# Kernel tuning notes

Measured on AMD Instinct MI355X. Metric: run time of the kernel, lower is better.

The kernel has to match this reference:

```python
import math
import jax, jax.numpy as jnp
import numpy as np

FS = 16000          # sample rate implied by undefined global `fs` in source
NFFT = 320          # win_len == frame_len
HOP = 160           # inc
C_SOUND = 340.0
ARRAY_DIS = 0.027


def _steering(F, n_ch, angle_deg):
    # h = conj(exp(-1j*2*pi*f_k * sensor * d * sin(theta)/c)) -> exp(+1j*...)
    f_k = np.arange(F) * (FS // NFFT)                      # integer bins * 50 Hz
    delay = np.arange(n_ch) * ARRAY_DIS * np.sin(angle_deg * np.pi / 180.0) / C_SOUND
    h = np.exp(1j * 2.0 * np.pi * f_k[:, None] * delay[None, :]).astype(np.complex64)
    return jnp.asarray(h)[..., None]                       # [F, C, 1]


def _stft(x, window):
    # x: [B, C, L] float32; torch.stft defaults: center=True, reflect pad
    pad = NFFT // 2
    xp = jnp.pad(x, ((0, 0), (0, 0), (pad, pad)), mode='reflect')
    T = 1 + (xp.shape[-1] - NFFT) // HOP
    idx = jnp.arange(T)[:, None] * HOP + jnp.arange(NFFT)[None, :]
    frames = xp[:, :, idx] * window                        # [B, C, T, NFFT]
    return jnp.fft.rfft(frames, axis=-1)                   # [B, C, T, F] complex64


def _istft(S):
    # S: [B, F, T] complex; torch.istft with default (rectangular) window
    frames = jnp.fft.irfft(jnp.moveaxis(S, 1, 2), n=NFFT, axis=-1)  # [B, T, NFFT]
    B, T, _ = frames.shape
    out_len = NFFT + HOP * (T - 1)
    idx = jnp.arange(T)[:, None] * HOP + jnp.arange(NFFT)[None, :]
    out = jnp.zeros((B, out_len), frames.dtype).at[:, idx].add(frames)
    wsum = jnp.zeros((out_len,), frames.dtype).at[idx.reshape(-1)].add(1.0)
    pad = NFFT // 2
    return (out / wsum)[:, pad:-pad]


def setup_inputs() -> dict:
    key = jax.random.key(0)
    B, L, C = 8, 160000, 4
    mc_wav = jax.random.normal(key, (B, L, C), dtype=jnp.float32)
    # torch.kaiser_window(320, periodic=True, beta=6)
    window = jnp.asarray(np.kaiser(NFFT + 1, 6.0)[:NFFT].astype(np.float32))
    return {"mc_wav": mc_wav, "window": window}


def reference(mc_wav, window):
    B, L, C = mc_wav.shape
    # pre-normalize: remove DC per channel, scale by per-batch global max-abs
    x = mc_wav - jnp.mean(mc_wav, axis=1, keepdims=True)
    x = x / jnp.max(jnp.abs(x), axis=(1, 2), keepdims=True)
    x = jnp.transpose(x, (0, 2, 1))                        # [B, C, L]

    S = _stft(x, window)                                   # [B, C, T, F]
    F = S.shape[-1]
    Xs = jnp.transpose(S, (2, 0, 3, 1))                    # [T, B, F, C] frames-first
    T = Xs.shape[0]

    h1 = _steering(F, C, -40.0)                            # [F, C, 1]
    h2 = _steering(F, C, 40.0)
    eye = jnp.eye(C, dtype=S.dtype)

    def beam(invR, h, X):
        num = jnp.einsum('bfcd,fdo->bfco', invR, h)        # invR @ h  [B,F,C,1]
        den = jnp.einsum('fco,bfco->bf', h.conj(), num)    # h^H invR h
        w = num[..., 0] / den[..., None]                   # [B, F, C]
        return jnp.einsum('bfc,bfc->bf', w.conj(), X)      # w^H X

    def step(RXX, inp):
        X, first = inp                                     # X: [B, F, C]
        outer = jnp.einsum('bfc,bfd->bfcd', X, X.conj())
        RXX = jnp.where(first, outer, 0.05 * RXX + 0.95 * outer)
        tr = jnp.trace(RXX, axis1=-2, axis2=-1)[..., None, None]
        invR = jnp.linalg.inv(RXX + (tr / C) * eye)        # diag-loaded inverse
        return RXX, (beam(invR, h1, X), beam(invR, h2, X))

    RXX0 = jnp.zeros((B, F, C, C), dtype=S.dtype)
    firsts = jnp.arange(T) == 0
    _, (s1, s2) = jax.lax.scan(step, RXX0, (Xs, firsts))

    S1 = jnp.transpose(s1, (1, 2, 0))                      # [B, F, T]
    S2 = jnp.transpose(s2, (1, 2, 0))
    return _istft(S1), _istft(S2)
```

## Files before the change

kernel.cpp:

```cpp
#include <hip/hip_runtime.h>
#include <hip/hip_bf16.h>
#include <math.h>

#define BB 8
#define LL 160000
#define CC 4
#define NFFT 320
#define HOP 160
#define FB 161
#define TT 1001
#define TP 1024
#define RBLK 128
#define PI_D 3.14159265358979323846
#define NPAD 160320

#define KWARM 4

#define GM 16016
#define KSEC 352
#define LDK 704
#define KT 11
#define NGEN (2*FB*CC + 384*640 + NFFT*LDK)

typedef __attribute__((ext_vector_type(8))) short bf16x8;
typedef __attribute__((ext_vector_type(4))) float f32x4;

__device__ __forceinline__ void ldsdma16(const short* g, short* l){
    __builtin_amdgcn_global_load_lds((const __attribute__((address_space(1))) void*)g,
                                     (__attribute__((address_space(3))) void*)l, 16, 0, 0);
}

__device__ __forceinline__ float2 cmulf(float2 a, float2 b){
    return make_float2(a.x*b.x - a.y*b.y, a.x*b.y + a.y*b.x);
}
__device__ __forceinline__ float2 cmulcj(float2 a, float2 b){
    return make_float2(a.x*b.x + a.y*b.y, a.y*b.x - a.x*b.y);
}
__device__ __forceinline__ float2 cjmul(float2 a, float2 b){
    return make_float2(a.x*b.x + a.y*b.y, a.x*b.y - a.y*b.x);
}
__device__ __forceinline__ float2 csub(float2 a, float2 b){ return make_float2(a.x-b.x, a.y-b.y); }
__device__ __forceinline__ float2 cscale(float2 a, float s){ return make_float2(a.x*s, a.y*s); }
__device__ __forceinline__ float2 cdivf(float2 a, float2 b){
    float inv = 1.0f/(b.x*b.x + b.y*b.y);
    return make_float2((a.x*b.x + a.y*b.y)*inv, (a.y*b.x - a.x*b.y)*inv);
}
__device__ __forceinline__ short bf_hi(float v){
    __hip_bfloat16 h = __float2bfloat16(v);
    short s; __builtin_memcpy(&s, &h, 2); return s;
}
__device__ __forceinline__ short bf_lo(float v){
    __hip_bfloat16 h = __float2bfloat16(v);
    float r = v - __bfloat162float(h);
    __hip_bfloat16 l = __float2bfloat16(r);
    short s; __builtin_memcpy(&s, &l, 2); return s;
}

__global__ __launch_bounds__(256) void k_genstats(const float* __restrict__ in, float* __restrict__ part,
        const float* __restrict__ win, float* __restrict__ htab,
        short* __restrict__ Bts, short* __restrict__ Bt){
    __shared__ float4 s4[256];
    __shared__ float4 mn4[256];
    __shared__ float4 mx4[256];
    int tid = threadIdx.x;
    if (blockIdx.x < BB*RBLK){
        int b = blockIdx.x / RBLK, chunk = blockIdx.x % RBLK;
        const float4* p = (const float4*)(in + (size_t)b*LL*CC);
        const int per = LL / RBLK;
        int start = chunk*per;
        float4 s  = make_float4(0.f,0.f,0.f,0.f);
        float4 mn = make_float4( 3.4e38f, 3.4e38f, 3.4e38f, 3.4e38f);
        float4 mx = make_float4(-3.4e38f,-3.4e38f,-3.4e38f,-3.4e38f);
        for (int i = start + tid; i < start + per; i += 256){
            float4 v = p[i];
            s.x += v.x; s.y += v.y; s.z += v.z; s.w += v.w;
            mn.x = fminf(mn.x, v.x); mn.y = fminf(mn.y, v.y); mn.z = fminf(mn.z, v.z); mn.w = fminf(mn.w, v.w);
            mx.x = fmaxf(mx.x, v.x); mx.y = fmaxf(mx.y, v.y); mx.z = fmaxf(mx.z, v.z); mx.w = fmaxf(mx.w, v.w);
        }
        s4[tid] = s; mn4[tid] = mn; mx4[tid] = mx;
        __syncthreads();
        for (int st = 128; st >= 1; st >>= 1){
            if (tid < st){
                float4 a = s4[tid], c = s4[tid+st];
                s4[tid] = make_float4(a.x+c.x, a.y+c.y, a.z+c.z, a.w+c.w);
                float4 d = mn4[tid], e = mn4[tid+st];
                mn4[tid] = make_float4(fminf(d.x,e.x), fminf(d.y,e.y), fminf(d.z,e.z), fminf(d.w,e.w));
                float4 f = mx4[tid], g = mx4[tid+st];
                mx4[tid] = make_float4(fmaxf(f.x,g.x), fmaxf(f.y,g.y), fmaxf(f.z,g.z), fmaxf(f.w,g.w));
            }
            __syncthreads();
        }
        if (tid == 0){
            float* dst = part + (size_t)(b*RBLK + chunk)*12;
            float4 a = s4[0], d = mn4[0], f = mx4[0];
            dst[0]=a.x; dst[1]=a.y; dst[2]=a.z; dst[3]=a.w;
            dst[4]=d.x; dst[5]=d.y; dst[6]=d.z; dst[7]=d.w;
            dst[8]=f.x; dst[9]=f.y; dst[10]=f.z; dst[11]=f.w;
        }
        return;
    }
    int gid = (blockIdx.x - BB*RBLK)*256 + tid;
    const float W0 = (float)(2.0*PI_D/320.0);
    if (gid < 2*FB*CC){
        int i = gid;
        int c = i & 3;
        int k = (i >> 2) % FB;
        int m = i / (FB*CC);
        double coef = 2.0*PI_D*50.0*0.027*sin(40.0*PI_D/180.0)/340.0;
        double sgn = (m == 0) ? -1.0 : 1.0;
        double ph = sgn*coef*(double)k*(double)c;
        double s, c2;
        sincos(ph, &s, &c2);
        ((float2*)htab)[i] = make_float2((float)c2, (float)s);
        return;
    }
    gid -= 2*FB*CC;
    if (gid < 384*640){
        int col = gid / 640, kk = gid % 640;
        int n = (kk >= 320) ? kk - 320 : kk;
        int sec = (kk >= 320) ? 1 : 0;
        float v = 0.f;
        if (col < 2*FB){
            int k = col >> 1;
            int mr = (k*n) % 320;
            float s, co; sincosf(W0*(float)mr, &s, &co);
            v = win[n] * ((col & 1) ? -s : co);
        }
        Bts[gid] = sec ? bf_lo(v) : bf_hi(v);
        return;
    }
    gid -= 384*640;
    if (gid < NFFT*LDK){
        int n = gid / LDK, kk = gid % LDK;
        int sec = (kk >= KSEC) ? 1 : 0;
        int kk2 = kk - (sec ? KSEC : 0);
        float v = 0.f;
        if (kk2 < 2*FB){
            int bin = kk2 >> 1;
            float c = ((bin == 0 || bin == 160) ? 1.0f : 2.0f) * (1.0f/320.0f);
            int mr = (bin*n) % 320;
            float s, co; sincosf(W0*(float)mr, &s, &co);
            v = (kk2 & 1) ? -c*s : c*co;
        }
        Bt[(size_t)n*LDK + kk] = sec ? bf_lo(v) : bf_hi(v);
    }
}

__global__ __launch_bounds__(128) void k_stats2(const float* __restrict__ part,
                                                float* __restrict__ mean, float* __restrict__ invmax){
    __shared__ float4 s4[128];
    __shared__ float4 mn4[128];
    __shared__ float4 mx4[128];
    int b = blockIdx.x, tid = threadIdx.x;
    const float* src = part + (size_t)(b*RBLK + tid)*12;
    s4[tid]  = make_float4(src[0], src[1], src[2], src[3]);
    mn4[tid] = make_float4(src[4], src[5], src[6], src[7]);
    mx4[tid] = make_float4(src[8], src[9], src[10], src[11]);
    __syncthreads();
    for (int st = 64; st >= 1; st >>= 1){
        if (tid < st){
            float4 a = s4[tid], c = s4[tid+st];
            s4[tid] = make_float4(a.x+c.x, a.y+c.y, a.z+c.z, a.w+c.w);
            float4 d = mn4[tid], e = mn4[tid+st];
            mn4[tid] = make_float4(fminf(d.x,e.x), fminf(d.y,e.y), fminf(d.z,e.z), fminf(d.w,e.w));
            float4 f = mx4[tid], g = mx4[tid+st];
            mx4[tid] = make_float4(fmaxf(f.x,g.x), fmaxf(f.y,g.y), fmaxf(f.z,g.z), fmaxf(f.w,g.w));
        }
        __syncthreads();
    }
    if (tid == 0){
        float4 sum = s4[0], mn = mn4[0], mx = mx4[0];
        float m0 = sum.x*(1.0f/LL), m1 = sum.y*(1.0f/LL), m2 = sum.z*(1.0f/LL), m3 = sum.w*(1.0f/LL);
        mean[b*4+0]=m0; mean[b*4+1]=m1; mean[b*4+2]=m2; mean[b*4+3]=m3;
        float a0 = fmaxf(mx.x - m0, m0 - mn.x);
        float a1 = fmaxf(mx.y - m1, m1 - mn.y);
        float a2 = fmaxf(mx.z - m2, m2 - mn.z);
        float a3 = fmaxf(mx.w - m3, m3 - mn.w);
        invmax[b] = 1.0f / fmaxf(fmaxf(a0, a1), fmaxf(a2, a3));
    }
}

__global__ __launch_bounds__(256) void k_anorm(const float* __restrict__ in,
        const float* __restrict__ mean, const float* __restrict__ invmax,
        short* __restrict__ Ahi, short* __restrict__ Alo){
    int gid = blockIdx.x*256 + threadIdx.x;
    if (gid >= BB*(NPAD/8)) return;
    int p8 = gid % (NPAD/8);
    int b  = gid / (NPAD/8);
    float4 mc = *(const float4*)&mean[b*4];
    float iv = invmax[b];
    const float4* px = (const float4*)(in + (size_t)b*LL*CC);
    bf16x8 h0{}, h1{}, h2{}, h3{}, l0{}, l1{}, l2{}, l3{};
    #pragma unroll
    for (int j = 0; j < 8; ++j){
        int p = p8*8 + j - 160;
        int m2 = p < 0 ? -p : (p >= LL ? 2*LL - 2 - p : p);
        float4 v = px[m2];
        float v0 = (v.x - mc.x)*iv, v1 = (v.y - mc.y)*iv;
        float v2 = (v.z - mc.z)*iv, v3 = (v.w - mc.w)*iv;
        h0[j] = bf_hi(v0); l0[j] = bf_lo(v0);
        h1[j] = bf_hi(v1); l1[j] = bf_lo(v1);
        h2[j] = bf_hi(v2); l2[j] = bf_lo(v2);
        h3[j] = bf_hi(v3); l3[j] = bf_lo(v3);
    }
    size_t o = (size_t)(b*4)*NPAD + (size_t)p8*8;
    *(bf16x8*)&Ahi[o]          = h0;  *(bf16x8*)&Alo[o]          = l0;
    *(bf16x8*)&Ahi[o +   NPAD] = h1;  *(bf16x8*)&Alo[o +   NPAD] = l1;
    *(bf16x8*)&Ahi[o + 2*NPAD] = h2;  *(bf16x8*)&Alo[o + 2*NPAD] = l2;
    *(bf16x8*)&Ahi[o + 3*NPAD] = h3;  *(bf16x8*)&Alo[o + 3*NPAD] = l3;
}

__global__ __launch_bounds__(512, 4) void k_gstft(const short* __restrict__ Ahi, const short* __restrict__ Alo,
        const short* __restrict__ Bts, float* __restrict__ S){
    __shared__ short stage[40960];
    int tid = threadIdx.x;
    int row0 = blockIdx.x*128;
    int col0 = blockIdx.y*192;
    int b  = row0 >> 12;
    int t0 = (row0 & 4095) >> 2;
    int wave = tid >> 6, lane = tid & 63;
    int wm = wave >> 1, wn = wave & 1;
    int l15 = lane & 15, quad = lane >> 4;
    int chunk = (tid & 3) ^ ((tid >> 3) & 3);
    int tq4 = tid >> 2;
    int rowA = tq4;
    int tls = t0 + (rowA >> 2); if (tls >= TT) tls = TT - 1;
    size_t gao = (size_t)(b*4 + (rowA & 3))*NPAD + (size_t)tls*160 + chunk*8;
    const short* src0 = Ahi + gao;
    const short* src1 = Alo + gao;
    const short* src2 = Bts + (size_t)(col0 + tq4)*640 + chunk*8;
    const short* src3 = (tid < 256)
        ? Bts + (size_t)(col0 + 128 + tq4)*640 + chunk*8
        : Bts + (size_t)(col0 + ((tid - 256) >> 2))*640 + 320 + chunk*8;
    const short* src4 = Bts + (size_t)(col0 + 64 + tq4)*640 + 320 + chunk*8;
    short* lw = stage + wave*512;
    int sw  = (l15 >> 1) & 3;
    int c0r = (quad ^ sw) * 8;
    int ra0 = (wm*32 + l15)*32 + c0r;
    int rbB = (wn*96 + l15)*32 + c0r;
    f32x4 c00 = {0.f,0.f,0.f,0.f}, c01 = c00, c02 = c00, c03 = c00, c04 = c00, c05 = c00;
    f32x4 c10 = c00, c11 = c00, c12 = c00, c13 = c00, c14 = c00, c15 = c00;

    #define STG(kt_, off_) do{ int ko_ = (kt_)*32; \
        ldsdma16(src0 + ko_, lw + (off_));          \
        ldsdma16(src1 + ko_, lw + (off_) + 4096);   \
        ldsdma16(src2 + ko_, lw + (off_) + 8192);   \
        ldsdma16(src3 + ko_, lw + (off_) + 12288);  \
        ldsdma16(src4 + ko_, lw + (off_) + 16384);  \
    }while(0)

    STG(0, 0);
    STG(1, 20480);
    #pragma unroll
    for (int kt = 0; kt < 10; ++kt){
        int offc = (kt & 1) ? 20480 : 0;
        if (kt < 9) asm volatile("s_waitcnt vmcnt(5)" ::: "memory");
        else        asm volatile("s_waitcnt vmcnt(0)" ::: "memory");
        __builtin_amdgcn_s_barrier();
        bf16x8 a0h = *(bf16x8*)&stage[offc + ra0];
        bf16x8 a1h = *(bf16x8*)&stage[offc + ra0 + 512];
        bf16x8 a0l = *(bf16x8*)&stage[offc + 4096 + ra0];
        bf16x8 a1l = *(bf16x8*)&stage[offc + 4096 + ra0 + 512];
        bf16x8 b0h = *(bf16x8*)&stage[offc + 8192 + rbB];
        bf16x8 b1h = *(bf16x8*)&stage[offc + 8192 + rbB + 512];
        bf16x8 b2h = *(bf16x8*)&stage[offc + 8192 + rbB + 1024];
        bf16x8 b3h = *(bf16x8*)&stage[offc + 8192 + rbB + 1536];
        bf16x8 b4h = *(bf16x8*)&stage[offc + 8192 + rbB + 2048];
        bf16x8 b5h = *(bf16x8*)&stage[offc + 8192 + rbB + 2560];
        c00 = __builtin_amdgcn_mfma_f32_16x16x32_bf16(a0h, b0h, c00, 0, 0, 0);
        c01 = __builtin_amdgcn_mfma_f32_16x16x32_bf16(a0h, b1h, c01, 0, 0, 0);
        c02 = __builtin_amdgcn_mfma_f32_16x16x32_bf16(a0h, b2h, c02, 0, 0, 0);
        c03 = __builtin_amdgcn_mfma_f32_16x16x32_bf16(a0h, b3h, c03, 0, 0, 0);
        c04 = __builtin_amdgcn_mfma_f32_16x16x32_bf16(a0h, b4h, c04, 0, 0, 0);
        c05 = __builtin_amdgcn_mfma_f32_16x16x32_bf16(a0h, b5h, c05, 0, 0, 0);
        c10 = __builtin_amdgcn_mfma_f32_16x16x32_bf16(a1h, b0h, c10, 0, 0, 0);
        c11 = __builtin_amdgcn_mfma_f32_16x16x32_bf16(a1h, b1h, c11, 0, 0, 0);
        c12 = __builtin_amdgcn_mfma_f32_16x16x32_bf16(a1h, b2h, c12, 0, 0, 0);
        c13 = __builtin_amdgcn_mfma_f32_16x16x32_bf16(a1h, b3h, c13, 0, 0, 0);
        c14 = __builtin_amdgcn_mfma_f32_16x16x32_bf16(a1h, b4h, c14, 0, 0, 0);
        c15 = __builtin_amdgcn_mfma_f32_16x16x32_bf16(a1h, b5h, c15, 0, 0, 0);
        c00 = __builtin_amdgcn_mfma_f32_16x16x32_bf16(a0l, b0h, c00, 0, 0, 0);
        c01 = __builtin_amdgcn_mfma_f32_16x16x32_bf16(a0l, b1h, c01, 0, 0, 0);
        c02 = __builtin_amdgcn_mfma_f32_16x16x32_bf16(a0l, b2h, c02, 0, 0, 0);
        c03 = __builtin_amdgcn_mfma_f32_16x16x32_bf16(a0l, b3h, c03, 0, 0, 0);
        c04 = __builtin_amdgcn_mfma_f32_16x16x32_bf16(a0l, b4h, c04, 0, 0, 0);
        c05 = __builtin_amdgcn_mfma_f32_16x16x32_bf16(a0l, b5h, c05, 0, 0, 0);
        c10 = __builtin_amdgcn_mfma_f32_16x16x32_bf16(a1l, b0h, c10, 0, 0, 0);
        c11 = __builtin_amdgcn_mfma_f32_16x16x32_bf16(a1l, b1h, c11, 0, 0, 0);
        c12 = __builtin_amdgcn_mfma_f32_16x16x32_bf16(a1l, b2h, c12, 0, 0, 0);
        c13 = __builtin_amdgcn_mfma_f32_16x16x32_bf16(a1l, b3h, c13, 0, 0, 0);
        c14 = __builtin_amdgcn_mfma_f32_16x16x32_bf16(a1l, b4h, c14, 0, 0, 0);
        c15 = __builtin_amdgcn_mfma_f32_16x16x32_bf16(a1l, b5h, c15, 0, 0, 0);
        bf16x8 b0l = *(bf16x8*)&stage[offc + 14336 + rbB];
        bf16x8 b1l = *(bf16x8*)&stage[offc + 14336 + rbB + 512];
        bf16x8 b2l = *(bf16x8*)&stage[offc + 14336 + rbB + 1024];
        bf16x8 b3l = *(bf16x8*)&stage[offc + 14336 + rbB + 1536];
        bf16x8 b4l = *(bf16x8*)&stage[offc + 14336 + rbB + 2048];
        bf16x8 b5l = *(bf16x8*)&stage[offc + 14336 + rbB + 2560];
        asm volatile("s_waitcnt lgkmcnt(0)" ::: "memory");
        __builtin_amdgcn_sched_barrier(0);
        __builtin_amdgcn_s_barrier();
        if (kt < 8) STG(kt+2, offc);
        c00 = __builtin_amdgcn_mfma_f32_16x16x32_bf16(a0h, b0l, c00, 0, 0, 0);
        c01 = __builtin_amdgcn_mfma_f32_16x16x32_bf16(a0h, b1l, c01, 0, 0, 0);
        c02 = __builtin_amdgcn_mfma_f32_16x16x32_bf16(a0h, b2l, c02, 0, 0, 0);
        c03 = __builtin_amdgcn_mfma_f32_16x16x32_bf16(a0h, b3l, c03, 0, 0, 0);
        c04 = __builtin_amdgcn_mfma_f32_16x16x32_bf16(a0h, b4l, c04, 0, 0, 0);
        c05 = __builtin_amdgcn_mfma_f32_16x16x32_bf16(a0h, b5l, c05, 0, 0, 0);
        c10 = __builtin_amdgcn_mfma_f32_16x16x32_bf16(a1h, b0l, c10, 0, 0, 0);
        c11 = __builtin_amdgcn_mfma_f32_16x16x32_bf16(a1h, b1l, c11, 0, 0, 0);
        c12 = __builtin_amdgcn_mfma_f32_16x16x32_bf16(a1h, b2l, c12, 0, 0, 0);
        c13 = __builtin_amdgcn_mfma_f32_16x16x32_bf16(a1h, b3l, c13, 0, 0, 0);
        c14 = __builtin_amdgcn_mfma_f32_16x16x32_bf16(a1h, b4l, c14, 0, 0, 0);
        c15 = __builtin_amdgcn_mfma_f32_16x16x32_bf16(a1h, b5l, c15, 0, 0, 0);
    }
    #undef STG
    int tq  = t0 + wm*8 + quad;
    int kgb = (col0 >> 1) + wn*48 + (l15 >> 1);
    int h   = l15 & 1;
    float4* S4 = (float4*)S;
    #define EPI(cf, i_, j_) do{ \
        int t = tq + 4*(i_); \
        int kg = kgb + 8*(j_); \
        if (t < TT && kg < FB){ \
            float p0 = __shfl_xor(cf[0], 1); \
            float p1 = __shfl_xor(cf[1], 1); \
            float p2 = __shfl_xor(cf[2], 1); \
            float p3 = __shfl_xor(cf[3], 1); \
            float4 v = h ? make_float4(p2, cf[2], p3, cf[3]) \
                         : make_float4(cf[0], p0, cf[1], p1); \
            S4[((size_t)((b*FB + kg)*2 + h))*TT + t] = v; \
        } \
    }while(0)
    EPI(c00, 0, 0); EPI(c01, 0, 1); EPI(c02, 0, 2); EPI(c03, 0, 3); EPI(c04, 0, 4); EPI(c05, 0, 5);
    EPI(c10, 1, 0); EPI(c11, 1, 1); EPI(c12, 1, 2); EPI(c13, 1, 3); EPI(c14, 1, 4); EPI(c15, 1, 5);
    #undef EPI
}

#define UPD(first) do{ \
    float aa = (first) ? 0.f : 0.05f; float wg = (first) ? 1.f : 0.95f; \
    float y0x=wg*x0.x, y0y=wg*x0.y, y1x=wg*x1.x, y1y=wg*x1.y; \
    float y2x=wg*x2.x, y2y=wg*x2.y, y3x=wg*x3.x, y3y=wg*x3.y; \
    d0 = aa*d0 + y0x*x0.x + y0y*x0.y; \
    d1 = aa*d1 + y1x*x1.x + y1y*x1.y; \
    d2 = aa*d2 + y2x*x2.x + y2y*x2.y; \
    d3 = aa*d3 + y3x*x3.x + y3y*x3.y; \
    r10.x = aa*r10.x + y1x*x0.x + y1y*x0.y;  r10.y = aa*r10.y + y1y*x0.x - y1x*x0.y; \
    r20.x = aa*r20.x + y2x*x0.x + y2y*x0.y;  r20.y = aa*r20.y + y2y*x0.x - y2x*x0.y; \
    r30.x = aa*r30.x + y3x*x0.x + y3y*x0.y;  r30.y = aa*r30.y + y3y*x0.x - y3x*x0.y; \
    r21.x = aa*r21.x + y2x*x1.x + y2y*x1.y;  r21.y = aa*r21.y + y2y*x1.x - y2x*x1.y; \
    r31.x = aa*r31.x + y3x*x1.x + y3y*x1.y;  r31.y = aa*r31.y + y3y*x1.x - y3x*x1.y; \
    r32.x = aa*r32.x + y3x*x2.x + y3y*x2.y;  r32.y = aa*r32.y + y3y*x2.x - y3x*x2.y; \
}while(0)

#define UPDQ do{ \
    d0 = 0.05f*d0 + x0.x*x0.x + x0.y*x0.y; \
    d1 = 0.05f*d1 + x1.x*x1.x + x1.y*x1.y; \
    d2 = 0.05f*d2 + x2.x*x2.x + x2.y*x2.y; \
    d3 = 0.05f*d3 + x3.x*x3.x + x3.y*x3.y; \
    r10.x = 0.05f*r10.x + x1.x*x0.x + x1.y*x0.y;  r10.y = 0.05f*r10.y + x1.y*x0.x - x1.x*x0.y; \
    r20.x = 0.05f*r20.x + x2.x*x0.x + x2.y*x0.y;  r20.y = 0.05f*r20.y + x2.y*x0.x - x2.x*x0.y; \
    r30.x = 0.05f*r30.x + x3.x*x0.x + x3.y*x0.y;  r30.y = 0.05f*r30.y + x3.y*x0.x - x3.x*x0.y; \
    r21.x = 0.05f*r21.x + x2.x*x1.x + x2.y*x1.y;  r21.y = 0.05f*r21.y + x2.y*x1.x - x2.x*x1.y; \
    r31.x = 0.05f*r31.x + x3.x*x1.x + x3.y*x1.y;  r31.y = 0.05f*r31.y + x3.y*x1.x - x3.x*x1.y; \
    r32.x = 0.05f*r32.x + x3.x*x2.x + x3.y*x2.y;  r32.y = 0.05f*r32.y + x3.y*x2.x - x3.x*x2.y; \
}while(0)

__global__ __launch_bounds__(512) void k_scan(const float* __restrict__ S, const float* __restrict__ htab,
                      short* __restrict__ S1, short* __restrict__ S2){
    __shared__ float4 tile[2016];
    int bf = blockIdx.x;
    int f  = bf % FB;
    int tid = threadIdx.x;
    const float4* P0 = (const float4*)S + (size_t)(bf*2)*TT;
    const float4* P1 = P0 + TT;
    for (int i = tid; i < 2*TT; i += 512){
        int tt = i >> 1;
        tile[i ^ ((i>>4)&7)] = (i & 1) ? P1[tt] : P0[tt];
    }
    __syncthreads();
    int t0 = tid*2;
    if (t0 < TT){
        const float2* hp = (const float2*)htab;
        float2 ha0 = hp[f*4+0], ha1 = hp[f*4+1], ha2 = hp[f*4+2], ha3 = hp[f*4+3];
        float2 hb0 = hp[(FB+f)*4+0], hb1 = hp[(FB+f)*4+1], hb2 = hp[(FB+f)*4+2], hb3 = hp[(FB+f)*4+3];
        float d0=0,d1=0,d2=0,d3=0;
        float2 r10={0,0}, r20={0,0}, r30={0,0}, r21={0,0}, r31={0,0}, r32={0,0};
        float2 x0, x1, x2, x3;
        #define LOADX(tau_) do{ int i0_ = 2*(tau_); \
            float4 v0_ = tile[i0_ ^ ((i0_>>4)&7)]; \
            float4 v1_ = tile[(i0_+1) ^ (((i0_+1)>>4)&7)]; \
            x0 = make_float2(v0_.x, v0_.y); x1 = make_float2(v0_.z, v0_.w); \
            x2 = make_float2(v1_.x, v1_.y); x3 = make_float2(v1_.z, v1_.w); \
        }while(0)
        bool qform = (t0 >= KWARM + 1);
        int ts = t0 - KWARM; if (ts < 0) ts = 0;
        if (qform){
            #pragma unroll
            for (int u = 0; u < KWARM; ++u){ LOADX(ts + u); UPDQ; }
        } else {
            for (int tau = 0; tau < t0; ++tau){ LOADX(tau); UPD(tau == 0); }
        }
        short4* S1g = (short4*)S1 + (size_t)bf*TT;
        short4* S2g = (short4*)S2 + (size_t)bf*TT;
        #pragma unroll
        for (int j = 0; j < 2; ++j){
            int t = t0 + j;
            if (t >= TT) break;
            LOADX(t);
            if (qform) UPDQ; else UPD(t == 0);
            float trc = d0 + d1 + d2 + d3;
            float lam = trc * 0.25f;
            float e0 = d0 + lam, e1 = d1 + lam, e2 = d2 + lam, e3 = d3 + lam;
            float detP = e0*e1 - (r10.x*r10.x + r10.y*r10.y);
            float2 w00 = csub(cscale(r20, e1), cmulf(r10, r21));
            float2 w01 = csub(cscale(r30, e1), cmulf(r10, r31));
            float2 w10 = csub(cscale(r21, e0), cjmul(r10, r20));
            float2 w11 = csub(cscale(r31, e0), cjmul(r10, r30));
            float2 va = cjmul(r30, w00), vb = cjmul(r31, w10);
            float2 V10 = make_float2(va.x + vb.x, -(va.y + vb.y));
            float reV00 = r20.x*w00.x + r20.y*w00.y + r21.x*w10.x + r21.y*w10.y;
            float reV11 = r30.x*w01.x + r30.y*w01.y + r31.x*w11.x + r31.y*w11.y;
            float t00 = detP*e2 - reV00;
            float t11 = detP*e3 - reV11;
            float2 t10 = csub(cscale(r32, detP), V10);
            float detT = t00*t11 - (t10.x*t10.x + t10.y*t10.y);
            #pragma unroll
            for (int m = 0; m < 2; ++m){
                float2 h0 = m ? hb0 : ha0;
                float2 h1 = m ? hb1 : ha1;
                float2 h2 = m ? hb2 : ha2;
                float2 h3 = m ? hb3 : ha3;
                float2 g0 = csub(cscale(h0, e1), cjmul(r10, h1));
                float2 g1 = csub(cscale(h1, e0), cmulf(r10, h0));
                float2 ta = cmulf(r20, g0), tb = cmulf(r21, g1);
                float2 hh0 = make_float2(detP*h2.x - ta.x - tb.x, detP*h2.y - ta.y - tb.y);
                ta = cmulf(r30, g0); tb = cmulf(r31, g1);
                float2 hh1 = make_float2(detP*h3.x - ta.x - tb.x, detP*h3.y - ta.y - tb.y);
                float2 y20 = csub(cscale(hh0, t11), cjmul(t10, hh1));
                float2 y21 = csub(cscale(hh1, t00), cmulf(t10, hh0));
                float2 u20 = cscale(y20, detP), u21 = cscale(y21, detP);
                ta = cmulcj(y20, r20); tb = cmulcj(y21, r30);
                float2 q0 = make_float2(detT*h0.x - ta.x - tb.x, detT*h0.y - ta.y - tb.y);
                ta = cmulcj(y20, r21); tb = cmulcj(y21, r31);
                float2 q1 = make_float2(detT*h1.x - ta.x - tb.x, detT*h1.y - ta.y - tb.y);
                float2 u10 = csub(cscale(q0, e1), cjmul(r10, q1));
                float2 u11 = csub(cscale(q1, e0), cmulf(r10, q0));
                float2 den = cjmul(h0, u10), tmp;
                tmp = cjmul(h1, u11); den.x += tmp.x; den.y += tmp.y;
                tmp = cjmul(h2, u20); den.x += tmp.x; den.y += tmp.y;
                tmp = cjmul(h3, u21); den.x += tmp.x; den.y += tmp.y;
                float2 num = cjmul(u10, x0);
                tmp = cjmul(u11, x1); num.x += tmp.x; num.y += tmp.y;
                tmp = cjmul(u20, x2); num.x += tmp.x; num.y += tmp.y;
                tmp = cjmul(u21, x3); num.x += tmp.x; num.y += tmp.y;
                float2 s = cdivf(num, make_float2(den.x, -den.y));
                short4 pk;
                pk.x = bf_hi(s.x); pk.y = bf_hi(s.y);
                pk.z = bf_lo(s.x); pk.w = bf_lo(s.y);
                if (m) S2g[t] = pk; else S1g[t] = pk;
            }
        }
        #undef LOADX
    }
}

__global__ __launch_bounds__(256) void k_pack(const short* __restrict__ S1, const short* __restrict__ S2,
                                              short* __restrict__ A){
    __shared__ short tile[32*708];
    int bid = blockIdx.x;
    int tb = bid & 31, rb = bid >> 5;
    int t0 = tb*32;
    int beam = rb >> 3, b = rb & 7;
    const short4* Sp = (const short4*)(beam ? S2 : S1) + (size_t)b*FB*TT;
    int tid = threadIdx.x;
    for (int idx = tid; idx < 32*176; idx += 256){
        int bin = idx >> 5, tq = idx & 31;
        int t = t0 + tq;
        short4 s = make_short4(0, 0, 0, 0);
        if (bin < FB && t < TT) s = Sp[(size_t)bin*TT + t];
        int c0 = 2*bin;
        tile[tq*708 + c0]            = s.x;
        tile[tq*708 + c0 + 1]        = s.y;
        tile[tq*708 + KSEC + c0]     = s.z;
        tile[tq*708 + KSEC + c0 + 1] = s.w;
    }
    __syncthreads();
    for (int idx = tid; idx < 32*176; idx += 256){
        int tq = idx / 176, k4 = idx % 176;
        int t = t0 + tq;
        if (t < TT)
            *(short4*)&A[(size_t)(rb*TT + t)*LDK + k4*4] = *(short4*)&tile[tq*708 + k4*4];
    }
}

__global__ __launch_bounds__(512, 4) void k_gemm(const short* __restrict__ A, const short* __restrict__ Bt,
                                                 float* __restrict__ C){
    __shared__ short sb2[24576];
    int tid = threadIdx.x;
    int row0 = blockIdx.y * 128;
    int col0 = blockIdx.x * 128;
    int wave = tid >> 6, lane = tid & 63;
    int wm = wave >> 1, wn = wave & 1;
    int l15 = lane & 15, quad = lane >> 4;
    bool wlive = (col0 + wn*64) < NFFT;
    int rowS  = wave*16 + (lane >> 2);
    int chunk = (lane & 3) ^ ((lane >> 3) & 3);
    int grS = row0 + rowS; if (grS >= GM) grS = GM - 1;
    int grB = col0 + rowS; if (grB >= NFFT) grB = NFFT - 1;
    const short* gA = A  + (size_t)grS*LDK + chunk*8;
    const short* gB = Bt + (size_t)grB*LDK + chunk*8;
    short* lA = sb2 + wave*512;
    int sw  = (l15 >> 1) & 3;
    int c0r = (quad ^ sw) * 8;
    int ra0 = (wm*32 + l15)*32 + c0r;
    int rb0 = (wn*64 + l15)*32 + c0r;
    f32x4 c00 = {0.f,0.f,0.f,0.f}, c01 = c00, c02 = c00, c03 = c00;
    f32x4 c10 = c00, c11 = c00, c12 = c00, c13 = c00;

    #define KOF(s_, ka_, kb_) { int sg_ = ((s_) >= 22) ? 2 : ((s_) >= 11) ? 1 : 0; \
        int kt_ = (s_) - sg_*11; \
        ka_ = ((sg_ == 1) ? KSEC : 0) + kt_*32; \
        kb_ = ((sg_ == 2) ? KSEC : 0) + kt_*32; }
    #define STG2(s_, off_) do{ int ka_, kb_; KOF(s_, ka_, kb_); \
        ldsdma16(gA + ka_, lA + (off_));        \
        ldsdma16(gB + kb_, lA + (off_) + 4096); \
    }while(0)

    STG2(0, 0);
    STG2(1, 8192);
    #pragma unroll
    for (int s = 0; s < 33; ++s){
        int offc = (s % 3) * 8192;
        if (s < 32) asm volatile("s_waitcnt vmcnt(2)" ::: "memory");
        else        asm volatile("s_waitcnt vmcnt(0)" ::: "memory");
        __builtin_amdgcn_s_barrier();
        if (s < 31) STG2(s+2, ((s+2) % 3) * 8192);
        bf16x8 a0{}, a1{}, b0{}, b1{}, b2{}, b3{};
        if (wlive){
            a0 = *(bf16x8*)&sb2[offc + ra0];
            a1 = *(bf16x8*)&sb2[offc + ra0 + 512];
            b0 = *(bf16x8*)&sb2[offc + 4096 + rb0];
            b1 = *(bf16x8*)&sb2[offc + 4096 + rb0 + 512];
            b2 = *(bf16x8*)&sb2[offc + 4096 + rb0 + 1024];
            b3 = *(bf16x8*)&sb2[offc + 4096 + rb0 + 1536];
            asm volatile("s_waitcnt lgkmcnt(0)" ::: "memory");
            __builtin_amdgcn_sched_barrier(0);
            c00 = __builtin_amdgcn_mfma_f32_16x16x32_bf16(a0, b0, c00, 0, 0, 0);
            c01 = __builtin_amdgcn_mfma_f32_16x16x32_bf16(a0, b1, c01, 0, 0, 0);
            c02 = __builtin_amdgcn_mfma_f32_16x16x32_bf16(a0, b2, c02, 0, 0, 0);
            c03 = __builtin_amdgcn_mfma_f32_16x16x32_bf16(a0, b3, c03, 0, 0, 0);
            c10 = __builtin_amdgcn_mfma_f32_16x16x32_bf16(a1, b0, c10, 0, 0, 0);
            c11 = __builtin_amdgcn_mfma_f32_16x16x32_bf16(a1, b1, c11, 0, 0, 0);
            c12 = __builtin_amdgcn_mfma_f32_16x16x32_bf16(a1, b2, c12, 0, 0, 0);
            c13 = __builtin_amdgcn_mfma_f32_16x16x32_bf16(a1, b3, c13, 0, 0, 0);
        }
    }
    #undef STG2
    #undef KOF
    if (wlive){
        #pragma unroll
        for (int r = 0; r < 4; ++r){
            int orow0 = row0 + wm*32 + quad*4 + r;
            int oc = col0 + wn*64 + l15;
            if (orow0 < GM){
                if (oc      < NFFT) C[(size_t)orow0*NFFT + oc]      = c00[r];
                if (oc + 16 < NFFT) C[(size_t)orow0*NFFT + oc + 16] = c01[r];
                if (oc + 32 < NFFT) C[(size_t)orow0*NFFT + oc + 32] = c02[r];
                if (oc + 48 < NFFT) C[(size_t)orow0*NFFT + oc + 48] = c03[r];
            }
            if (orow0 + 16 < GM){
                if (oc      < NFFT) C[(size_t)(orow0+16)*NFFT + oc]      = c10[r];
                if (oc + 16 < NFFT) C[(size_t)(orow0+16)*NFFT + oc + 16] = c11[r];
                if (oc + 32 < NFFT) C[(size_t)(orow0+16)*NFFT + oc + 32] = c12[r];
                if (oc + 48 < NFFT) C[(size_t)(orow0+16)*NFFT + oc + 48] = c13[r];
            }
        }
    }
}

__global__ __launch_bounds__(256) void k_ola(const float* __restrict__ frames, float* __restrict__ out){
    int gid = blockIdx.x*256 + threadIdx.x;
    if (gid >= 2*BB*(LL/4)) return;
    int o4 = (gid % (LL/4))*4;
    int rb = gid / (LL/4);
    int i  = o4 + HOP;
    int t1 = i / HOP;
    int r  = i - t1*HOP;
    const float4* fb = (const float4*)(frames + (size_t)rb*TT*NFFT);
    float4 a = fb[(t1*NFFT + r) >> 2];
    float4 b = fb[((t1-1)*NFFT + r + HOP) >> 2];
    ((float4*)out)[gid] = make_float4(0.5f*(a.x+b.x), 0.5f*(a.y+b.y), 0.5f*(a.z+b.z), 0.5f*(a.w+b.w));
}

extern "C" void kernel_launch(void* const* d_in, const int* in_sizes, int n_in,
                              void* d_out, int out_size, void* d_ws, size_t ws_size,
                              hipStream_t stream){
    const float* in  = (const float*)d_in[0];
    const float* win = (const float*)d_in[1];
    float* ws = (float*)d_ws;
    float* mean   = ws;
    float* invmax = ws + 32;
    float* htab   = ws + 48;
    float* S1     = ws + 3072;
    size_t nS1 = (size_t)2*BB*FB*TT;
    float* S2 = S1 + nS1;
    float* S  = S2 + nS1;
    float* part = S1;
    short* Ahi = (short*)S1;
    short* Alo = Ahi + (size_t)BB*CC*NPAD;
    short* Bts = (short*)d_out;
    short* Bt  = (short*)((float*)d_out + 131072);
    short* A  = (short*)S;
    float* frames = S1;

    k_genstats<<<dim3(BB*RBLK + (NGEN + 255)/256), dim3(256), 0, stream>>>(in, part, win, htab, Bts, Bt);
    k_stats2<<<dim3(BB), dim3(128), 0, stream>>>(part, mean, invmax);
    k_anorm<<<dim3((BB*(NPAD/8) + 255)/256), dim3(256), 0, stream>>>(in, mean, invmax, Ahi, Alo);
    k_gstft<<<dim3(BB*TP*CC/128, 2), dim3(512), 0, stream>>>(Ahi, Alo, Bts, S);
    k_scan<<<dim3(BB*FB), dim3(512), 0, stream>>>(S, htab, (short*)S1, (short*)S2);
    k_pack<<<dim3(512), dim3(256), 0, stream>>>((const short*)S1, (const short*)S2, A);
    k_gemm<<<dim3((NFFT + 127)/128, (GM + 127)/128), dim3(512), 0, stream>>>(A, Bt, frames);
    k_ola<<<dim3((2*BB*(LL/4) + 255)/256), dim3(256), 0, stream>>>(frames, (float*)d_out);
}
```

Measured before the change: 189.0 us.

## Fuse overlap-add into GEMM epilogue via atomics and move Bt generation into pack

The separate overlap-add kernel is removed. The inverse-DFT GEMM epilogue now atomically adds half-scaled frame samples straight into the zeroed output, and the pack kernel gains extra blocks that zero the output and build the inverse-DFT basis table. This drops one launch and the write and re-read of the full frame buffer. In exchange it adds float atomics to global memory and a non-deterministic summation order, and the basis table is generated later in a different workspace location.

```diff
diff --git a/kernel.cpp b/kernel.cpp
--- a/kernel.cpp
+++ b/kernel.cpp
@@ -20,7 +20,10 @@
 #define KSEC 352
 #define LDK 704
 #define KT 11
-#define NGEN (2*FB*CC + 384*640 + NFFT*LDK)
+#define NGEN (2*FB*CC + 384*640)
+#define PACK_BLK 512
+#define ZERO_BLK 2500
+#define GENBT_BLK 880
 
 typedef __attribute__((ext_vector_type(8))) short bf16x8;
 typedef __attribute__((ext_vector_type(4))) float f32x4;
@@ -57,8 +60,7 @@
 }
 
 __global__ __launch_bounds__(256) void k_genstats(const float* __restrict__ in, float* __restrict__ part,
-        const float* __restrict__ win, float* __restrict__ htab,
-        short* __restrict__ Bts, short* __restrict__ Bt){
+        const float* __restrict__ win, float* __restrict__ htab, short* __restrict__ Bts){
     __shared__ float4 s4[256];
     __shared__ float4 mn4[256];
     __shared__ float4 mx4[256];
@@ -127,22 +129,6 @@
             v = win[n] * ((col & 1) ? -s : co);
         }
         Bts[gid] = sec ? bf_lo(v) : bf_hi(v);
-        return;
-    }
-    gid -= 384*640;
-    if (gid < NFFT*LDK){
-        int n = gid / LDK, kk = gid % LDK;
-        int sec = (kk >= KSEC) ? 1 : 0;
-        int kk2 = kk - (sec ? KSEC : 0);
-        float v = 0.f;
-        if (kk2 < 2*FB){
-            int bin = kk2 >> 1;
-            float c = ((bin == 0 || bin == 160) ? 1.0f : 2.0f) * (1.0f/320.0f);
-            int mr = (bin*n) % 320;
-            float s, co; sincosf(W0*(float)mr, &s, &co);
-            v = (kk2 & 1) ? -c*s : c*co;
-        }
-        Bt[(size_t)n*LDK + kk] = sec ? bf_lo(v) : bf_hi(v);
     }
 }
 
@@ -466,36 +452,61 @@
 }
 
 __global__ __launch_bounds__(256) void k_pack(const short* __restrict__ S1, const short* __restrict__ S2,
-                                              short* __restrict__ A){
-    __shared__ short tile[32*708];
+                                              short* __restrict__ A, float* __restrict__ outz,
+                                              short* __restrict__ Bt, const float* __restrict__ win){
     int bid = blockIdx.x;
-    int tb = bid & 31, rb = bid >> 5;
-    int t0 = tb*32;
-    int beam = rb >> 3, b = rb & 7;
-    const short4* Sp = (const short4*)(beam ? S2 : S1) + (size_t)b*FB*TT;
     int tid = threadIdx.x;
-    for (int idx = tid; idx < 32*176; idx += 256){
-        int bin = idx >> 5, tq = idx & 31;
-        int t = t0 + tq;
-        short4 s = make_short4(0, 0, 0, 0);
-        if (bin < FB && t < TT) s = Sp[(size_t)bin*TT + t];
-        int c0 = 2*bin;
-        tile[tq*708 + c0]            = s.x;
-        tile[tq*708 + c0 + 1]        = s.y;
-        tile[tq*708 + KSEC + c0]     = s.z;
-        tile[tq*708 + KSEC + c0 + 1] = s.w;
-    }
-    __syncthreads();
-    for (int idx = tid; idx < 32*176; idx += 256){
-        int tq = idx / 176, k4 = idx % 176;
-        int t = t0 + tq;
-        if (t < TT)
-            *(short4*)&A[(size_t)(rb*TT + t)*LDK + k4*4] = *(short4*)&tile[tq*708 + k4*4];
+    if (bid < PACK_BLK){
+        __shared__ short tile[32*708];
+        int tb = bid & 31, rb = bid >> 5;
+        int t0 = tb*32;
+        int beam = rb >> 3, b = rb & 7;
+        const short4* Sp = (const short4*)(beam ? S2 : S1) + (size_t)b*FB*TT;
+        for (int idx = tid; idx < 32*176; idx += 256){
+            int bin = idx >> 5, tq = idx & 31;
+            int t = t0 + tq;
+            short4 s = make_short4(0, 0, 0, 0);
+            if (bin < FB && t < TT) s = Sp[(size_t)bin*TT + t];
+            int c0 = 2*bin;
+            tile[tq*708 + c0]            = s.x;
+            tile[tq*708 + c0 + 1]        = s.y;
+            tile[tq*708 + KSEC + c0]     = s.z;
+            tile[tq*708 + KSEC + c0 + 1] = s.w;
+        }
+        __syncthreads();
+        for (int idx = tid; idx < 32*176; idx += 256){
+            int tq = idx / 176, k4 = idx % 176;
+            int t = t0 + tq;
+            if (t < TT)
+                *(short4*)&A[(size_t)(rb*TT + t)*LDK + k4*4] = *(short4*)&tile[tq*708 + k4*4];
+        }
+        return;
+    }
+    if (bid < PACK_BLK + ZERO_BLK){
+        int g = (bid - PACK_BLK)*256 + tid;
+        ((float4*)outz)[g] = make_float4(0.f, 0.f, 0.f, 0.f);
+        return;
+    }
+    int gid = (bid - PACK_BLK - ZERO_BLK)*256 + tid;
+    if (gid < NFFT*LDK){
+        const float W0 = (float)(2.0*PI_D/320.0);
+        int n = gid / LDK, kk = gid % LDK;
+        int sec = (kk >= KSEC) ? 1 : 0;
+        int kk2 = kk - (sec ? KSEC : 0);
+        float v = 0.f;
+        if (kk2 < 2*FB){
+            int bin = kk2 >> 1;
+            float c = ((bin == 0 || bin == 160) ? 1.0f : 2.0f) * (1.0f/320.0f);
+            int mr = (bin*n) % 320;
+            float s, co; sincosf(W0*(float)mr, &s, &co);
+            v = (kk2 & 1) ? -c*s : c*co;
+        }
+        Bt[(size_t)n*LDK + kk] = sec ? bf_lo(v) : bf_hi(v);
     }
 }
 
 __global__ __launch_bounds__(512, 4) void k_gemm(const short* __restrict__ A, const short* __restrict__ Bt,
-                                                 float* __restrict__ C){
+                                                 float* __restrict__ out){
     __shared__ short sb2[24576];
     int tid = threadIdx.x;
     int row0 = blockIdx.y * 128;
@@ -559,38 +570,28 @@
     #undef STG2
     #undef KOF
     if (wlive){
+        #define OST(mm_, cc_, vv_) do{ \
+            if ((mm_) < GM && (cc_) < NFFT){ \
+                int rb_ = (mm_) / TT, t_ = (mm_) - rb_*TT; \
+                int ii_ = t_*HOP + (cc_) - HOP; \
+                if (ii_ >= 0 && ii_ < LL) \
+                    atomicAdd(&out[(size_t)rb_*LL + ii_], 0.5f*(vv_)); \
+            } }while(0)
         #pragma unroll
         for (int r = 0; r < 4; ++r){
-            int orow0 = row0 + wm*32 + quad*4 + r;
+            int m0 = row0 + wm*32 + quad*4 + r;
             int oc = col0 + wn*64 + l15;
-            if (orow0 < GM){
-                if (oc      < NFFT) C[(size_t)orow0*NFFT + oc]      = c00[r];
-                if (oc + 16 < NFFT) C[(size_t)orow0*NFFT + oc + 16] = c01[r];
-                if (oc + 32 < NFFT) C[(size_t)orow0*NFFT + oc + 32] = c02[r];
-                if (oc + 48 < NFFT) C[(size_t)orow0*NFFT + oc + 48] = c03[r];
-            }
-            if (orow0 + 16 < GM){
-                if (oc      < NFFT) C[(size_t)(orow0+16)*NFFT + oc]      = c10[r];
-                if (oc + 16 < NFFT) C[(size_t)(orow0+16)*NFFT + oc + 16] = c11[r];
-                if (oc + 32 < NFFT) C[(size_t)(orow0+16)*NFFT + oc + 32] = c12[r];
-                if (oc + 48 < NFFT) C[(size_t)(orow0+16)*NFFT + oc + 48] = c13[r];
-            }
-        }
-    }
-}
-
-__global__ __launch_bounds__(256) void k_ola(const float* __restrict__ frames, float* __restrict__ out){
-    int gid = blockIdx.x*256 + threadIdx.x;
-    if (gid >= 2*BB*(LL/4)) return;
-    int o4 = (gid % (LL/4))*4;
-    int rb = gid / (LL/4);
-    int i  = o4 + HOP;
-    int t1 = i / HOP;
-    int r  = i - t1*HOP;
-    const float4* fb = (const float4*)(frames + (size_t)rb*TT*NFFT);
-    float4 a = fb[(t1*NFFT + r) >> 2];
-    float4 b = fb[((t1-1)*NFFT + r + HOP) >> 2];
-    ((float4*)out)[gid] = make_float4(0.5f*(a.x+b.x), 0.5f*(a.y+b.y), 0.5f*(a.z+b.z), 0.5f*(a.w+b.w));
+            OST(m0,    oc,      c00[r]);
+            OST(m0,    oc + 16, c01[r]);
+            OST(m0,    oc + 32, c02[r]);
+            OST(m0,    oc + 48, c03[r]);
+            OST(m0+16, oc,      c10[r]);
+            OST(m0+16, oc + 16, c11[r]);
+            OST(m0+16, oc + 32, c12[r]);
+            OST(m0+16, oc + 48, c13[r]);
+        }
+        #undef OST
+    }
 }
 
 extern "C" void kernel_launch(void* const* d_in, const int* in_sizes, int n_in,
@@ -610,16 +611,15 @@
     short* Ahi = (short*)S1;
     short* Alo = Ahi + (size_t)BB*CC*NPAD;
     short* Bts = (short*)d_out;
-    short* Bt  = (short*)((float*)d_out + 131072);
-    short* A  = (short*)S;
-    float* frames = S1;
-
-    k_genstats<<<dim3(BB*RBLK + (NGEN + 255)/256), dim3(256), 0, stream>>>(in, part, win, htab, Bts, Bt);
+    short* A   = (short*)S;
+    short* Bt  = (short*)(S + 8000000);
+
+    k_genstats<<<dim3(BB*RBLK + (NGEN + 255)/256), dim3(256), 0, stream>>>(in, part, win, htab, Bts);
     k_stats2<<<dim3(BB), dim3(128), 0, stream>>>(part, mean, invmax);
     k_anorm<<<dim3((BB*(NPAD/8) + 255)/256), dim3(256), 0, stream>>>(in, mean, invmax, Ahi, Alo);
     k_gstft<<<dim3(BB*TP*CC/128, 2), dim3(512), 0, stream>>>(Ahi, Alo, Bts, S);
     k_scan<<<dim3(BB*FB), dim3(512), 0, stream>>>(S, htab, (short*)S1, (short*)S2);
-    k_pack<<<dim3(512), dim3(256), 0, stream>>>((const short*)S1, (const short*)S2, A);
-    k_gemm<<<dim3((NFFT + 127)/128, (GM + 127)/128), dim3(512), 0, stream>>>(A, Bt, frames);
-    k_ola<<<dim3((2*BB*(LL/4) + 255)/256), dim3(256), 0, stream>>>(frames, (float*)d_out);
-}
+    k_pack<<<dim3(PACK_BLK + ZERO_BLK + GENBT_BLK), dim3(256), 0, stream>>>(
+        (const short*)S1, (const short*)S2, A, (float*)d_out, Bt, win);
+    k_gemm<<<dim3((NFFT + 127)/128, (GM + 127)/128), dim3(512), 0, stream>>>(A, Bt, (float*)d_out);
+}
```

After: 188.9 us. Within noise of the previous version (-0.0%).
